# Kernel optimization log

Hardware: AMD Instinct MI355X
Metric: run time of the kernel (lower is better)

## Reference

```python
import jax, jax.numpy as jnp
import numpy as np

B, T, V, E_DIM, M_DIM, H = 32, 256, 10000, 300, 128, 256


def setup_inputs() -> dict:
    key = jax.random.key(0)
    ks = jax.random.split(key, 8)
    sc = 0.05
    words = jax.random.randint(ks[0], (B, T), 0, V)            # int token ids, 0 = pad
    midis = jax.random.normal(ks[1], (B, T, M_DIM), dtype=jnp.float32)
    E  = jax.random.normal(ks[2], (V, E_DIM), dtype=jnp.float32) * sc   # embedding table
    Wm = jax.random.normal(ks[3], (M_DIM, E_DIM), dtype=jnp.float32) * sc  # midi Dense
    bm = jnp.zeros((E_DIM,), jnp.float32)
    Wx = jax.random.normal(ks[4], (E_DIM, 3 * H), dtype=jnp.float32) * sc  # GRU input kernel [z|r|h]
    bx = jnp.zeros((3 * H,), jnp.float32)
    U  = jax.random.normal(ks[5], (H, 3 * H), dtype=jnp.float32) * sc      # GRU recurrent kernel
    bu = jnp.zeros((3 * H,), jnp.float32)                                  # recurrent bias (reset_after)
    Wo = jax.random.normal(ks[6], (H, V), dtype=jnp.float32) * sc          # output Dense
    bo = jnp.zeros((V,), jnp.float32)
    return {"words": words, "midis": midis, "E": E, "Wm": Wm, "bm": bm,
            "Wx": Wx, "bx": bx, "U": U, "bu": bu, "Wo": Wo, "bo": bo}


def _gru_masked(x, mask, Wx, bx, U, bu):
    """Keras GRU (reset_after=True) with mask carry-through. x: [B,T,E], mask: [B,T] bool."""
    gx = x @ Wx + bx                      # [B,T,3H] precomputed input gates
    gx_t = jnp.swapaxes(gx, 0, 1)         # [T,B,3H]
    m_t = mask.T                          # [T,B]
    h0 = jnp.zeros((x.shape[0], H), x.dtype)

    def step(h, inp):
        g, m = inp
        gh = h @ U + bu                   # [B,3H]
        xz, xr, xn = jnp.split(g, 3, axis=-1)
        hz, hr, hn = jnp.split(gh, 3, axis=-1)
        z = jax.nn.sigmoid(xz + hz)
        r = jax.nn.sigmoid(xr + hr)
        n = jnp.tanh(xn + r * hn)         # reset_after: r applied to recurrent projection
        h_new = z * h + (1.0 - z) * n
        h_new = jnp.where(m[:, None], h_new, h)  # masked step: carry state/output
        return h_new, h_new

    h_last, seq = jax.lax.scan(step, h0, (gx_t, m_t))
    return jnp.swapaxes(seq, 0, 1), h_last  # [B,T,H], [B,H]


def reference(words, midis, E, Wm, bm, Wx, bx, U, bu, Wo, bo):
    mask = words != 0                      # Embedding(mask_zero=True).compute_mask
    x = E[words] + (midis @ Wm + bm)       # [B,T,E] fused embedding + dense add
    seq, _ = _gru_masked(x, mask, Wx, bx, U, bu)
    return seq @ Wo + bo                   # [B,T,V] logits
```

## Files before the change

### kernel.cpp

```cpp
#include <hip/hip_runtime.h>
#include <hip/hip_fp16.h>

typedef unsigned short ushort_t;
typedef short bf16x8 __attribute__((ext_vector_type(8)));
typedef float f32x4 __attribute__((ext_vector_type(4)));
typedef _Float16 h2v __attribute__((ext_vector_type(2)));

#define B_SZ 32
#define T_SZ 256
#define V_SZ 10000
#define E_DIM 300
#define M_DIM 128
#define H_SZ 256

__device__ __forceinline__ ushort_t f2bf(float f) {
  unsigned u = __float_as_uint(f);
  unsigned r = u + 0x7fffu + ((u >> 16) & 1u);
  return (ushort_t)(r >> 16);
}

__global__ void k_cast_bf16(const float* __restrict__ in, ushort_t* __restrict__ out, int n) {
  int i = blockIdx.x * blockDim.x + threadIdx.x;
  if (i < n) out[i] = f2bf(in[i]);
}

template <int MODE>
__global__ void k_transpose_cast(const float* __restrict__ in, ushort_t* __restrict__ out,
                                 int R, int C, int Rp, int Cp) {
  __shared__ float tile[32][33];
  int c0 = blockIdx.x * 32, r0 = blockIdx.y * 32;
  int tx = threadIdx.x, ty = threadIdx.y;
#pragma unroll
  for (int i = 0; i < 32; i += 8) {
    int r = r0 + ty + i, c = c0 + tx;
    tile[ty + i][tx] = (r < R && c < C) ? in[(size_t)r * C + c] : 0.f;
  }
  __syncthreads();
#pragma unroll
  for (int i = 0; i < 32; i += 8) {
    int c = c0 + ty + i, r = r0 + tx;
    if (c < Cp && r < Rp) {
      float v = tile[tx][ty + i];
      if (MODE == 0) {
        out[(size_t)c * Rp + r] = f2bf(v);
      } else {
        __half h = __float2half(v);
        out[(size_t)c * Rp + r] = *(ushort_t*)&h;
      }
    }
  }
}

__global__ void k_xfuse(const float* __restrict__ xtmp, const float* __restrict__ E,
                        const int* __restrict__ words, ushort_t* __restrict__ xb) {
  int m = blockIdx.x;
  int kp = threadIdx.x;
  int w = words[m];
  float v = 0.f;
  if (kp < E_DIM) v = xtmp[(size_t)m * 320 + kp] + E[(size_t)w * E_DIM + kp];
  xb[(size_t)m * 320 + kp] = f2bf(v);
}

__global__ __launch_bounds__(256, 2) void k_gemm_bt(
    const ushort_t* __restrict__ A, const ushort_t* __restrict__ BT,
    const float* __restrict__ bias, float* __restrict__ C,
    int M, int K, int Nreal, int ldc) {
  __shared__ __align__(16) char smem[32768];
  char* As = smem;
  char* Bs = smem + 16384;
  const int tid = threadIdx.x;
  const int lane = tid & 63;
  const int w = tid >> 6;
  const int wr = w >> 1, wc = w & 1;
  const int m0 = blockIdx.x * 128;
  const int n0 = blockIdx.y * 128;

  f32x4 acc[4][4];
#pragma unroll
  for (int i = 0; i < 4; ++i)
#pragma unroll
    for (int j = 0; j < 4; ++j) acc[i][j] = (f32x4){0.f, 0.f, 0.f, 0.f};

  const int srow = tid >> 3;
  const int sc16 = tid & 7;

  for (int k0 = 0; k0 < K; k0 += 64) {
    __syncthreads();
#pragma unroll
    for (int it = 0; it < 4; ++it) {
      int row = srow + it * 32;
      int slot = sc16 ^ (row & 7);
      bf16x8 va = *(const bf16x8*)(A + (size_t)(m0 + row) * K + k0 + sc16 * 8);
      *(bf16x8*)(As + row * 128 + (slot << 4)) = va;
      bf16x8 vb = *(const bf16x8*)(BT + (size_t)(n0 + row) * K + k0 + sc16 * 8);
      *(bf16x8*)(Bs + row * 128 + (slot << 4)) = vb;
    }
    __syncthreads();

    bf16x8 af[4][2], bfr[4][2];
#pragma unroll
    for (int mi = 0; mi < 4; ++mi) {
      int r = wr * 64 + mi * 16 + (lane & 15);
#pragma unroll
      for (int kk = 0; kk < 2; ++kk) {
        int c16 = kk * 4 + (lane >> 4);
        af[mi][kk] = *(const bf16x8*)(As + r * 128 + ((c16 ^ (r & 7)) << 4));
      }
    }
#pragma unroll
    for (int ni = 0; ni < 4; ++ni) {
      int r = wc * 64 + ni * 16 + (lane & 15);
#pragma unroll
      for (int kk = 0; kk < 2; ++kk) {
        int c16 = kk * 4 + (lane >> 4);
        bfr[ni][kk] = *(const bf16x8*)(Bs + r * 128 + ((c16 ^ (r & 7)) << 4));
      }
    }
#pragma unroll
    for (int mi = 0; mi < 4; ++mi)
#pragma unroll
      for (int ni = 0; ni < 4; ++ni)
#pragma unroll
        for (int kk = 0; kk < 2; ++kk)
          acc[mi][ni] = __builtin_amdgcn_mfma_f32_16x16x32_bf16(af[mi][kk], bfr[ni][kk],
                                                                acc[mi][ni], 0, 0, 0);
  }

  const int rbase = m0 + wr * 64 + (lane >> 4) * 4;
  const int cbase = n0 + wc * 64 + (lane & 15);
#pragma unroll
  for (int ni = 0; ni < 4; ++ni) {
    int n = cbase + ni * 16;
    if (n < Nreal) {
      float bn = bias[n];
#pragma unroll
      for (int mi = 0; mi < 4; ++mi) {
#pragma unroll
        for (int rg = 0; rg < 4; ++rg) {
          int mrow = rbase + mi * 16 + rg;
          C[(size_t)mrow * ldc + n] = acc[mi][ni][rg] + bn;
        }
      }
    }
  }
}

__global__ __launch_bounds__(768, 3) void k_gru(
    const float* __restrict__ gx, const ushort_t* __restrict__ UT,
    const float* __restrict__ bu, const int* __restrict__ words,
    ushort_t* __restrict__ seqb) {
  const int b = blockIdx.x;
  const int j = threadIdx.x;
  __shared__ __align__(16) _Float16 hbuf[2][H_SZ];
  __shared__ float rbuf[H_SZ];
  __shared__ float hnbuf[H_SZ];
  __shared__ int words_s[T_SZ];

  const h2v* Uc = (const h2v*)(UT + (size_t)j * H_SZ);
  h2v Ur[128];
#pragma unroll
  for (int k = 0; k < 128; ++k) Ur[k] = Uc[k];
  const float bu_j = bu[j];

  if (j < H_SZ) hbuf[0][j] = (_Float16)0.f;
  if (j < T_SZ) words_s[j] = words[b * T_SZ + j];
  __syncthreads();

  const float* gxp = gx + (size_t)b * T_SZ * 768;
  float gxv = gxp[j];
  float xn = (j < H_SZ) ? gxp[2 * H_SZ + j] : 0.f;
  float h_old = 0.f;
  int p = 0;

  for (int t = 0; t < T_SZ; ++t) {
    float gxv_n = 0.f, xn_n = 0.f;
    if (t + 1 < T_SZ) {
      const float* gxr1 = gxp + (size_t)(t + 1) * 768;
      gxv_n = gxr1[j];
      if (j < H_SZ) xn_n = gxr1[2 * H_SZ + j];
    }

    const float4* hb4 = (const float4*)hbuf[p];
    float a0 = 0.f, a1 = 0.f, a2 = 0.f, a3 = 0.f;
#pragma unroll
    for (int k4 = 0; k4 < 32; ++k4) {
      float4 hv = hb4[k4];
      const h2v* hp = (const h2v*)(&hv);
      a0 = __builtin_amdgcn_fdot2(Ur[4 * k4 + 0], hp[0], a0, false);
      a1 = __builtin_amdgcn_fdot2(Ur[4 * k4 + 1], hp[1], a1, false);
      a2 = __builtin_amdgcn_fdot2(Ur[4 * k4 + 2], hp[2], a2, false);
      a3 = __builtin_amdgcn_fdot2(Ur[4 * k4 + 3], hp[3], a3, false);
    }
    float gh = (a0 + a1) + (a2 + a3) + bu_j;

    float z = 0.f;
    if (j >= 2 * H_SZ) {
      hnbuf[j - 2 * H_SZ] = gh;
    } else if (j >= H_SZ) {
      rbuf[j - H_SZ] = 1.f / (1.f + __expf(-(gxv + gh)));
    } else {
      z = 1.f / (1.f + __expf(-(gxv + gh)));
    }
    __syncthreads();
    if (j < H_SZ) {
      float ni = xn + rbuf[j] * hnbuf[j];
      float n = 2.f / (1.f + __expf(-2.f * ni)) - 1.f;
      float hnew = (words_s[t] != 0) ? (z * h_old + (1.f - z) * n) : h_old;
      h_old = hnew;
      seqb[((size_t)b * T_SZ + t) * H_SZ + j] = f2bf(hnew);
      hbuf[p ^ 1][j] = (_Float16)hnew;
    }
    __syncthreads();
    gxv = gxv_n;
    xn = xn_n;
    p ^= 1;
  }
}

extern "C" void kernel_launch(void* const* d_in, const int* in_sizes, int n_in,
                              void* d_out, int out_size, void* d_ws, size_t ws_size,
                              hipStream_t stream) {
  const int*   words = (const int*)d_in[0];
  const float* midis = (const float*)d_in[1];
  const float* E     = (const float*)d_in[2];
  const float* Wm    = (const float*)d_in[3];
  const float* bm    = (const float*)d_in[4];
  const float* Wx    = (const float*)d_in[5];
  const float* bx    = (const float*)d_in[6];
  const float* U     = (const float*)d_in[7];
  const float* bu    = (const float*)d_in[8];
  const float* Wo    = (const float*)d_in[9];
  const float* bo    = (const float*)d_in[10];
  float* out = (float*)d_out;

  const int MT = B_SZ * T_SZ;
  size_t off = 0;
  auto alloc = [&](size_t bytes) -> void* {
    void* p = (char*)d_ws + off;
    off += (bytes + 255) & ~(size_t)255;
    return p;
  };
  ushort_t* mid_b = (ushort_t*)alloc((size_t)MT * 128 * 2);
  ushort_t* WmT   = (ushort_t*)alloc((size_t)384 * 128 * 2);
  float*    xtmp  = (float*)   alloc((size_t)MT * 320 * 4);
  ushort_t* x_b   = (ushort_t*)alloc((size_t)MT * 320 * 2);
  ushort_t* WxT   = (ushort_t*)alloc((size_t)768 * 320 * 2);
  float*    gx    = (float*)   alloc((size_t)MT * 768 * 4);
  ushort_t* UT    = (ushort_t*)alloc((size_t)768 * 256 * 2);
  ushort_t* seq_b = (ushort_t*)alloc((size_t)MT * 256 * 2);
  ushort_t* WoT   = (ushort_t*)alloc((size_t)10112 * 256 * 2);
  (void)ws_size;

  k_cast_bf16<<<(MT * 128 + 255) / 256, 256, 0, stream>>>(midis, mid_b, MT * 128);
  k_transpose_cast<0><<<dim3(12, 4),  dim3(32, 8), 0, stream>>>(Wm, WmT, 128, 300, 128, 384);
  k_transpose_cast<0><<<dim3(24, 10), dim3(32, 8), 0, stream>>>(Wx, WxT, 300, 768, 320, 768);
  k_transpose_cast<0><<<dim3(316, 8), dim3(32, 8), 0, stream>>>(Wo, WoT, 256, 10000, 256, 10112);
  k_transpose_cast<1><<<dim3(24, 8),  dim3(32, 8), 0, stream>>>(U, UT, 256, 768, 256, 768);

  k_gemm_bt<<<dim3(64, 3), 256, 0, stream>>>(mid_b, WmT, bm, xtmp, MT, 128, 300, 320);
  k_xfuse<<<MT, 320, 0, stream>>>(xtmp, E, words, x_b);
  k_gemm_bt<<<dim3(64, 6), 256, 0, stream>>>(x_b, WxT, bx, gx, MT, 320, 768, 768);
  k_gru<<<B_SZ, 768, 0, stream>>>(gx, UT, bu, words, seq_b);
  k_gemm_bt<<<dim3(64, 79), 256, 0, stream>>>(seq_b, WoT, bo, out, MT, 256, 10000, 10000);
}
```

Baseline: 502.9 us.

## Compute all three GRU gates per thread to drop one barrier per step

The GRU kernel now uses 256 threads per block instead of 768. Each thread keeps its z, r and n columns of the recurrent weights in registers (384 packed half2 values) and computes all three gate dot products itself. This removes the shared-memory exchange of r and hn and one __syncthreads per timestep. In exchange, each step issues three times more dot-product work per thread on fewer waves, and register pressure becomes very high, which risks spills into scratch memory.

```diff
diff --git a/kernel.cpp b/kernel.cpp
--- a/kernel.cpp
+++ b/kernel.cpp
@@ -145,74 +145,88 @@
   }
 }
 
-__global__ __launch_bounds__(768, 3) void k_gru(
+__global__ __launch_bounds__(256) void k_gru(
     const float* __restrict__ gx, const ushort_t* __restrict__ UT,
     const float* __restrict__ bu, const int* __restrict__ words,
     ushort_t* __restrict__ seqb) {
   const int b = blockIdx.x;
   const int j = threadIdx.x;
   __shared__ __align__(16) _Float16 hbuf[2][H_SZ];
-  __shared__ float rbuf[H_SZ];
-  __shared__ float hnbuf[H_SZ];
   __shared__ int words_s[T_SZ];
 
-  const h2v* Uc = (const h2v*)(UT + (size_t)j * H_SZ);
-  h2v Ur[128];
-#pragma unroll
-  for (int k = 0; k < 128; ++k) Ur[k] = Uc[k];
-  const float bu_j = bu[j];
-
-  if (j < H_SZ) hbuf[0][j] = (_Float16)0.f;
-  if (j < T_SZ) words_s[j] = words[b * T_SZ + j];
+  h2v uz[128], ur[128], un[128];
+  {
+    const h2v* pz = (const h2v*)(UT + (size_t)j * H_SZ);
+    const h2v* pr = (const h2v*)(UT + (size_t)(H_SZ + j) * H_SZ);
+    const h2v* pn = (const h2v*)(UT + (size_t)(2 * H_SZ + j) * H_SZ);
+#pragma unroll
+    for (int k = 0; k < 128; ++k) uz[k] = pz[k];
+#pragma unroll
+    for (int k = 0; k < 128; ++k) ur[k] = pr[k];
+#pragma unroll
+    for (int k = 0; k < 128; ++k) un[k] = pn[k];
+  }
+  const float buz = bu[j];
+  const float bur = bu[H_SZ + j];
+  const float bun = bu[2 * H_SZ + j];
+
+  hbuf[0][j] = (_Float16)0.f;
+  words_s[j] = words[b * T_SZ + j];
   __syncthreads();
 
   const float* gxp = gx + (size_t)b * T_SZ * 768;
-  float gxv = gxp[j];
-  float xn = (j < H_SZ) ? gxp[2 * H_SZ + j] : 0.f;
+  float gxz = gxp[j];
+  float gxr = gxp[H_SZ + j];
+  float gxn = gxp[2 * H_SZ + j];
   float h_old = 0.f;
   int p = 0;
 
   for (int t = 0; t < T_SZ; ++t) {
-    float gxv_n = 0.f, xn_n = 0.f;
+    float gxz_n = 0.f, gxr_n = 0.f, gxn_n = 0.f;
     if (t + 1 < T_SZ) {
-      const float* gxr1 = gxp + (size_t)(t + 1) * 768;
-      gxv_n = gxr1[j];
-      if (j < H_SZ) xn_n = gxr1[2 * H_SZ + j];
+      const float* g1 = gxp + (size_t)(t + 1) * 768;
+      gxz_n = g1[j];
+      gxr_n = g1[H_SZ + j];
+      gxn_n = g1[2 * H_SZ + j];
     }
 
     const float4* hb4 = (const float4*)hbuf[p];
-    float a0 = 0.f, a1 = 0.f, a2 = 0.f, a3 = 0.f;
+    float az0 = 0.f, az1 = 0.f, az2 = 0.f, az3 = 0.f;
+    float ar0 = 0.f, ar1 = 0.f, ar2 = 0.f, ar3 = 0.f;
+    float an0 = 0.f, an1 = 0.f, an2 = 0.f, an3 = 0.f;
 #pragma unroll
     for (int k4 = 0; k4 < 32; ++k4) {
       float4 hv = hb4[k4];
       const h2v* hp = (const h2v*)(&hv);
-      a0 = __builtin_amdgcn_fdot2(Ur[4 * k4 + 0], hp[0], a0, false);
-      a1 = __builtin_amdgcn_fdot2(Ur[4 * k4 + 1], hp[1], a1, false);
-      a2 = __builtin_amdgcn_fdot2(Ur[4 * k4 + 2], hp[2], a2, false);
-      a3 = __builtin_amdgcn_fdot2(Ur[4 * k4 + 3], hp[3], a3, false);
-    }
-    float gh = (a0 + a1) + (a2 + a3) + bu_j;
-
-    float z = 0.f;
-    if (j >= 2 * H_SZ) {
-      hnbuf[j - 2 * H_SZ] = gh;
-    } else if (j >= H_SZ) {
-      rbuf[j - H_SZ] = 1.f / (1.f + __expf(-(gxv + gh)));
-    } else {
-      z = 1.f / (1.f + __expf(-(gxv + gh)));
-    }
+      az0 = __builtin_amdgcn_fdot2(uz[4 * k4 + 0], hp[0], az0, false);
+      ar0 = __builtin_amdgcn_fdot2(ur[4 * k4 + 0], hp[0], ar0, false);
+      an0 = __builtin_amdgcn_fdot2(un[4 * k4 + 0], hp[0], an0, false);
+      az1 = __builtin_amdgcn_fdot2(uz[4 * k4 + 1], hp[1], az1, false);
+      ar1 = __builtin_amdgcn_fdot2(ur[4 * k4 + 1], hp[1], ar1, false);
+      an1 = __builtin_amdgcn_fdot2(un[4 * k4 + 1], hp[1], an1, false);
+      az2 = __builtin_amdgcn_fdot2(uz[4 * k4 + 2], hp[2], az2, false);
+      ar2 = __builtin_amdgcn_fdot2(ur[4 * k4 + 2], hp[2], ar2, false);
+      an2 = __builtin_amdgcn_fdot2(un[4 * k4 + 2], hp[2], an2, false);
+      az3 = __builtin_amdgcn_fdot2(uz[4 * k4 + 3], hp[3], az3, false);
+      ar3 = __builtin_amdgcn_fdot2(ur[4 * k4 + 3], hp[3], ar3, false);
+      an3 = __builtin_amdgcn_fdot2(un[4 * k4 + 3], hp[3], an3, false);
+    }
+    float hz = (az0 + az1) + (az2 + az3) + buz;
+    float hr = (ar0 + ar1) + (ar2 + ar3) + bur;
+    float hn = (an0 + an1) + (an2 + an3) + bun;
+
+    float z = 1.f / (1.f + __expf(-(gxz + hz)));
+    float r = 1.f / (1.f + __expf(-(gxr + hr)));
+    float nv = 2.f / (1.f + __expf(-2.f * (gxn + r * hn))) - 1.f;
+    float hnew = (words_s[t] != 0) ? (z * h_old + (1.f - z) * nv) : h_old;
+    h_old = hnew;
+    seqb[((size_t)b * T_SZ + t) * H_SZ + j] = f2bf(hnew);
+    hbuf[p ^ 1][j] = (_Float16)hnew;
     __syncthreads();
-    if (j < H_SZ) {
-      float ni = xn + rbuf[j] * hnbuf[j];
-      float n = 2.f / (1.f + __expf(-2.f * ni)) - 1.f;
-      float hnew = (words_s[t] != 0) ? (z * h_old + (1.f - z) * n) : h_old;
-      h_old = hnew;
-      seqb[((size_t)b * T_SZ + t) * H_SZ + j] = f2bf(hnew);
-      hbuf[p ^ 1][j] = (_Float16)hnew;
-    }
-    __syncthreads();
-    gxv = gxv_n;
-    xn = xn_n;
+
+    gxz = gxz_n;
+    gxr = gxr_n;
+    gxn = gxn_n;
     p ^= 1;
   }
 }
@@ -260,6 +274,6 @@
   k_gemm_bt<<<dim3(64, 3), 256, 0, stream>>>(mid_b, WmT, bm, xtmp, MT, 128, 300, 320);
   k_xfuse<<<MT, 320, 0, stream>>>(xtmp, E, words, x_b);
   k_gemm_bt<<<dim3(64, 6), 256, 0, stream>>>(x_b, WxT, bx, gx, MT, 320, 768, 768);
-  k_gru<<<B_SZ, 768, 0, stream>>>(gx, UT, bu, words, seq_b);
+  k_gru<<<B_SZ, 256, 0, stream>>>(gx, UT, bu, words, seq_b);
   k_gemm_bt<<<dim3(64, 79), 256, 0, stream>>>(seq_b, WoT, bo, out, MT, 256, 10000, 10000);
 }
```

Measured after the change: 679.2 us. +35.1%, slower.
